# Kernel tuning notes

Measured on AMD Instinct MI355X. Metric: run time of the kernel, lower is better.

The kernel has to match this reference:

```python
import jax, jax.numpy as jnp
import numpy as np

B, T, D, H = 2, 2048, 1024, 16
HD = D // H  # head_dim = 64

def setup_inputs() -> dict:
    key = jax.random.key(0)
    ks = jax.random.split(key, 5)
    s = 0.02
    return {
        "x": jax.random.normal(ks[0], (B, T, D), dtype=jnp.float32),
        "w_qkv": jax.random.normal(ks[1], (3 * D, D), dtype=jnp.float32) * s,
        "b_qkv": jax.random.normal(ks[2], (3 * D,), dtype=jnp.float32) * s,
        "w_proj": jax.random.normal(ks[3], (D, D), dtype=jnp.float32) * s,
        "b_proj": jax.random.normal(ks[4], (D,), dtype=jnp.float32) * s,
    }

def reference(x, w_qkv, b_qkv, w_proj, b_proj):
    b, t, c = x.shape
    h, hd = H, HD
    scale = hd ** -0.5
    # qkv projection (torch Linear: x @ W^T + b)
    qkv = x @ w_qkv.T + b_qkv                      # [b, t, 3c]
    q, k, v = jnp.split(qkv, 3, axis=-1)
    # b t (h d) -> b h t d
    reshape = lambda z: z.reshape(b, t, h, hd).transpose(0, 2, 1, 3)
    q, k, v = reshape(q), reshape(k), reshape(v)
    scores = jnp.einsum("bhqd,bhkd->bhqk", q, k) * scale  # [b, h, t, t]
    causal = jnp.triu(jnp.ones((t, t), dtype=bool), k=1)   # True above diag
    scores = jnp.where(causal[None, None], -jnp.inf, scores)
    attn = jax.nn.softmax(scores, axis=-1)
    out = jnp.einsum("bhqk,bhkd->bhqd", attn, v)            # [b, h, t, d]
    out = out.transpose(0, 2, 1, 3).reshape(b, t, c)        # b h t d -> b t (h d)
    return out @ w_proj.T + b_proj
```

## Files before the change

### kernel.cpp

```cpp
#include <hip/hip_runtime.h>
#include <hip/hip_bf16.h>

#define Bq 2
#define Tq 2048
#define Dq 1024
#define Hq 16
#define HDq 64

typedef __attribute__((ext_vector_type(8))) short short8;
typedef __attribute__((ext_vector_type(4))) float f32x4;

__device__ __forceinline__ unsigned short f2bf(float f) {
  union { float f; unsigned int i; } v; v.f = f;
  unsigned int r = v.i + 0x7fffu + ((v.i >> 16) & 1u);
  return (unsigned short)(r >> 16);
}
__device__ __forceinline__ unsigned short f2bf_fast(float f) {
  union { float f; unsigned int i; } v; v.f = f;
  return (unsigned short)((v.i + 0x8000u) >> 16);
}

__device__ __forceinline__ short8 cvt8(const float* __restrict__ g) {
  const float4* gp = (const float4*)g;
  float4 x0 = gp[0], x1 = gp[1];
  short8 v;
  v[0] = (short)f2bf(x0.x); v[1] = (short)f2bf(x0.y);
  v[2] = (short)f2bf(x0.z); v[3] = (short)f2bf(x0.w);
  v[4] = (short)f2bf(x1.x); v[5] = (short)f2bf(x1.y);
  v[6] = (short)f2bf(x1.z); v[7] = (short)f2bf(x1.w);
  return v;
}

__device__ __forceinline__ void async_cp16(const void* g, void* l) {
  __builtin_amdgcn_global_load_lds(
      (const __attribute__((address_space(1))) void*)g,
      (__attribute__((address_space(3))) void*)l, 16, 0, 0);
}

constexpr int NXC = (Bq * Tq * Dq) / 8;
constexpr int NW1C = (3 * Dq * Dq) / 8;
constexpr int NW2C = (Dq * Dq) / 8;

__global__ __launch_bounds__(256)
void cvt_all(const float* __restrict__ x, const float* __restrict__ w1,
             const float* __restrict__ w2, unsigned short* __restrict__ xo,
             unsigned short* __restrict__ w1o, unsigned short* __restrict__ w2o)
{
  int i = blockIdx.x * 256 + threadIdx.x;
  const float* src; unsigned short* dst; int j;
  if (i < NXC)              { src = x;  dst = xo;  j = i; }
  else if (i < NXC + NW1C)  { src = w1; dst = w1o; j = i - NXC; }
  else                      { src = w2; dst = w2o; j = i - NXC - NW1C; }
  *(short8*)&dst[(size_t)j * 8] = cvt8(src + (size_t)j * 8);
}

template<int EPI, int BN_>
__global__ __launch_bounds__(256)
void gemm_bt(const unsigned short* __restrict__ Ab, const unsigned short* __restrict__ Wb,
             const float* __restrict__ bias, float* __restrict__ outp,
             int K, int N,
             unsigned short* __restrict__ qo, unsigned short* __restrict__ ko,
             unsigned short* __restrict__ vo)
{
  constexpr int WN = BN_ / 2;
  constexpr int NJ = WN / 16;
  constexpr int NAI = 4;
  constexpr int NBI = BN_ / 32;
  __shared__ unsigned short As[2][2 * 128 * 32];
  __shared__ unsigned short Bs[2][2 * BN_ * 32];

  const int t = threadIdx.x;
  const int lane = t & 63, w = t >> 6;
  const int m0 = blockIdx.y * 128, n0 = blockIdx.x * BN_;
  const int fr = lane & 15, qd = lane >> 4;
  const int wm = (w >> 1) * 64, wn = (w & 1) * WN;

  f32x4 acc[4][NJ] = {};
  const int NIT = K / 64;

  #pragma unroll
  for (int j = 0; j < NAI; j++) {
    int G = j * 256 + t;
    int panel = G >> 9, rowg = (G >> 2) & 127, colg = G & 3;
    async_cp16(Ab + (size_t)(m0 + rowg) * K + panel * 32 + colg * 8, &As[0][G * 8]);
  }
  #pragma unroll
  for (int j = 0; j < NBI; j++) {
    int G = j * 256 + t;
    int panel = G / (BN_ * 4), rowg = (G / 4) % BN_, colg = G & 3;
    async_cp16(Wb + (size_t)(n0 + rowg) * K + panel * 32 + colg * 8, &Bs[0][G * 8]);
  }

  for (int i = 0; i < NIT; i++) {
    const int cur = i & 1;
    __syncthreads();
    if (i + 1 < NIT) {
      const int nxt = cur ^ 1;
      const int k0 = (i + 1) * 64;
      #pragma unroll
      for (int j = 0; j < NAI; j++) {
        int G = j * 256 + t;
        int panel = G >> 9, rowg = (G >> 2) & 127, colg = G & 3;
        async_cp16(Ab + (size_t)(m0 + rowg) * K + k0 + panel * 32 + colg * 8, &As[nxt][G * 8]);
      }
      #pragma unroll
      for (int j = 0; j < NBI; j++) {
        int G = j * 256 + t;
        int panel = G / (BN_ * 4), rowg = (G / 4) % BN_, colg = G & 3;
        async_cp16(Wb + (size_t)(n0 + rowg) * K + k0 + panel * 32 + colg * 8, &Bs[nxt][G * 8]);
      }
    }
    #pragma unroll
    for (int kh = 0; kh < 2; kh++) {
      short8 af[4], bf[NJ];
      #pragma unroll
      for (int ib = 0; ib < 4; ib++)
        af[ib] = *(const short8*)&As[cur][kh * 4096 + (wm + ib * 16 + fr) * 32 + qd * 8];
      #pragma unroll
      for (int jb = 0; jb < NJ; jb++)
        bf[jb] = *(const short8*)&Bs[cur][kh * (BN_ * 32) + (wn + jb * 16 + fr) * 32 + qd * 8];
      #pragma unroll
      for (int ib = 0; ib < 4; ib++)
        #pragma unroll
        for (int jb = 0; jb < NJ; jb++)
          acc[ib][jb] = __builtin_amdgcn_mfma_f32_16x16x32_bf16(af[ib], bf[jb], acc[ib][jb], 0, 0, 0);
    }
  }

  #pragma unroll
  for (int jb = 0; jb < NJ; jb++) {
    int col = n0 + wn + jb * 16 + fr;
    float bv = bias[col];
    if (EPI == 0) {
      int which = col >> 10;
      int rem = col & 1023;
      int hh = rem >> 6, dd = rem & 63;
      #pragma unroll
      for (int ib = 0; ib < 4; ib++) {
        int row4 = m0 + wm + ib * 16 + qd * 4;
        int bb = row4 >> 11, tt = row4 & (Tq - 1);
        if (which == 2) {
          unsigned lo = (unsigned)f2bf(acc[ib][jb][0] + bv)
                      | ((unsigned)f2bf(acc[ib][jb][1] + bv) << 16);
          unsigned hi = (unsigned)f2bf(acc[ib][jb][2] + bv)
                      | ((unsigned)f2bf(acc[ib][jb][3] + bv) << 16);
          uint2 pk; pk.x = lo; pk.y = hi;
          *(uint2*)&vo[((size_t)(bb * Hq + hh) * HDq + dd) * Tq + tt] = pk;
        } else {
          unsigned short* dst = (which == 0) ? qo : ko;
          #pragma unroll
          for (int r = 0; r < 4; r++)
            dst[((size_t)(bb * Hq + hh) * Tq + tt + r) * HDq + dd] = f2bf(acc[ib][jb][r] + bv);
        }
      }
    } else {
      #pragma unroll
      for (int ib = 0; ib < 4; ib++)
        #pragma unroll
        for (int r = 0; r < 4; r++) {
          int row = m0 + wm + ib * 16 + qd * 4 + r;
          outp[(size_t)row * N + col] = acc[ib][jb][r] + bv;
        }
    }
  }
}

constexpr int AP = 72;

template<bool DIAG>
__device__ __forceinline__ void strip_one(
    const short8 aq0, const short8 aq1,
    const short8 (&bk)[4][2], const short8 (&bv)[4][2], const short8 ones,
    unsigned short* __restrict__ PsRow, int fr, int qd, int qbase,
    f32x4 (&oacc)[4], f32x4& lacc, float SCL)
{
  f32x4 s4[4] = {};
  #pragma unroll
  for (int nb = 0; nb < 4; nb++) {
    s4[nb] = __builtin_amdgcn_mfma_f32_16x16x32_bf16(aq0, bk[nb][0], s4[nb], 0, 0, 0);
    s4[nb] = __builtin_amdgcn_mfma_f32_16x16x32_bf16(aq1, bk[nb][1], s4[nb], 0, 0, 0);
  }
  #pragma unroll
  for (int nb = 0; nb < 4; nb++)
    #pragma unroll
    for (int reg = 0; reg < 4; reg++) {
      float pv = exp2f(s4[nb][reg] * SCL);
      if (DIAG && (nb * 16 + fr) > (qbase + reg)) pv = 0.f;
      PsRow[(qd * 4 + reg) * AP + nb * 16 + fr] = f2bf_fast(pv);
    }
  short8 ap0 = *(const short8*)&PsRow[fr * AP + qd * 8];
  short8 ap1 = *(const short8*)&PsRow[fr * AP + 32 + qd * 8];
  lacc = __builtin_amdgcn_mfma_f32_16x16x32_bf16(ap0, ones, lacc, 0, 0, 0);
  lacc = __builtin_amdgcn_mfma_f32_16x16x32_bf16(ap1, ones, lacc, 0, 0, 0);
  #pragma unroll
  for (int db = 0; db < 4; db++) {
    oacc[db] = __builtin_amdgcn_mfma_f32_16x16x32_bf16(ap0, bv[db][0], oacc[db], 0, 0, 0);
    oacc[db] = __builtin_amdgcn_mfma_f32_16x16x32_bf16(ap1, bv[db][1], oacc[db], 0, 0, 0);
  }
}

template<bool SMALLDIAG>
__device__ __forceinline__ void strip_dual(
    const short8 (&aqB)[2], const short8 (&aqA)[2],
    const short8 (&bk)[4][2], const short8 (&bv)[4][2], const short8 ones,
    unsigned short* __restrict__ PsB, unsigned short* __restrict__ PsA,
    int fr, int qd, int qbase,
    f32x4 (&oB)[4], f32x4& lB, f32x4 (&oA)[4], f32x4& lA, float SCL)
{
  f32x4 sB[4] = {}, sA[4] = {};
  #pragma unroll
  for (int nb = 0; nb < 4; nb++) {
    sB[nb] = __builtin_amdgcn_mfma_f32_16x16x32_bf16(aqB[0], bk[nb][0], sB[nb], 0, 0, 0);
    sA[nb] = __builtin_amdgcn_mfma_f32_16x16x32_bf16(aqA[0], bk[nb][0], sA[nb], 0, 0, 0);
  }
  #pragma unroll
  for (int nb = 0; nb < 4; nb++) {
    sB[nb] = __builtin_amdgcn_mfma_f32_16x16x32_bf16(aqB[1], bk[nb][1], sB[nb], 0, 0, 0);
    sA[nb] = __builtin_amdgcn_mfma_f32_16x16x32_bf16(aqA[1], bk[nb][1], sA[nb], 0, 0, 0);
  }
  #pragma unroll
  for (int nb = 0; nb < 4; nb++)
    #pragma unroll
    for (int reg = 0; reg < 4; reg++) {
      float pvB = exp2f(sB[nb][reg] * SCL);
      float pvA = exp2f(sA[nb][reg] * SCL);
      if (SMALLDIAG && (nb * 16 + fr) > (qbase + reg)) pvA = 0.f;
      PsB[(qd * 4 + reg) * AP + nb * 16 + fr] = f2bf_fast(pvB);
      PsA[(qd * 4 + reg) * AP + nb * 16 + fr] = f2bf_fast(pvA);
    }
  short8 apB0 = *(const short8*)&PsB[fr * AP + qd * 8];
  short8 apB1 = *(const short8*)&PsB[fr * AP + 32 + qd * 8];
  short8 apA0 = *(const short8*)&PsA[fr * AP + qd * 8];
  short8 apA1 = *(const short8*)&PsA[fr * AP + 32 + qd * 8];
  lB = __builtin_amdgcn_mfma_f32_16x16x32_bf16(apB0, ones, lB, 0, 0, 0);
  lA = __builtin_amdgcn_mfma_f32_16x16x32_bf16(apA0, ones, lA, 0, 0, 0);
  lB = __builtin_amdgcn_mfma_f32_16x16x32_bf16(apB1, ones, lB, 0, 0, 0);
  lA = __builtin_amdgcn_mfma_f32_16x16x32_bf16(apA1, ones, lA, 0, 0, 0);
  #pragma unroll
  for (int db = 0; db < 4; db++) {
    oB[db] = __builtin_amdgcn_mfma_f32_16x16x32_bf16(apB0, bv[db][0], oB[db], 0, 0, 0);
    oA[db] = __builtin_amdgcn_mfma_f32_16x16x32_bf16(apA0, bv[db][0], oA[db], 0, 0, 0);
  }
  #pragma unroll
  for (int db = 0; db < 4; db++) {
    oB[db] = __builtin_amdgcn_mfma_f32_16x16x32_bf16(apB1, bv[db][1], oB[db], 0, 0, 0);
    oA[db] = __builtin_amdgcn_mfma_f32_16x16x32_bf16(apA1, bv[db][1], oA[db], 0, 0, 0);
  }
}

__global__ __launch_bounds__(256, 2)
void attn_fwd(const unsigned short* __restrict__ qb, const unsigned short* __restrict__ kb,
              const unsigned short* __restrict__ vtb, unsigned short* __restrict__ ab)
{
  __shared__ unsigned short Ks[2][64 * 64];
  __shared__ unsigned short Vts[2][64 * 64];
  __shared__ unsigned short Ps[128 * AP];

  const int t = threadIdx.x, w = t >> 6, lane = t & 63;
  const int fr = lane & 15, qd = lane >> 4;
  const int p = blockIdx.x;
  const int bh = blockIdx.y;
  const int sB = 31 - p;
  const int sA = p;
  const int s0t[2] = { sB * 64, sA * 64 };
  const int ktB = sB;
  const int qbase = w * 16 + qd * 4;

  short8 aq[2][2];
  #pragma unroll
  for (int tl = 0; tl < 2; tl++) {
    const unsigned short* Qg = qb + ((size_t)bh * Tq + s0t[tl]) * HDq;
    #pragma unroll
    for (int c = 0; c < 2; c++)
      aq[tl][c] = *(const short8*)(Qg + (w * 16 + fr) * 64 + c * 32 + qd * 8);
  }

  const unsigned short* Kbh = kb + (size_t)bh * Tq * HDq;
  const unsigned short* Vbh = vtb + (size_t)bh * HDq * Tq;

  const int off0 = ((qd ^ (fr & 7)) * 8);
  const int off1 = off0 ^ 32;

  const int G0 = 2 * w * 64 + lane, G1 = G0 + 64;
  const int r0 = G0 >> 3, g0 = (G0 & 7) ^ (r0 & 7);
  const int r1 = G1 >> 3, g1 = (G1 & 7) ^ (r1 & 7);

  short8 ones;
  #pragma unroll
  for (int j = 0; j < 8; j++) ones[j] = (short)0x3F80;

  f32x4 oacc[2][4] = {};
  f32x4 lacc[2] = {};
  const float SCL = 0.125f * 1.44269504088896f;

  unsigned short* PsB = &Ps[(0 * 64 + w * 16) * AP];
  unsigned short* PsA = &Ps[(1 * 64 + w * 16) * AP];

  async_cp16(Kbh + (size_t)r0 * 64 + g0 * 8, &Ks[0][G0 * 8]);
  async_cp16(Vbh + (size_t)r0 * Tq + g0 * 8, &Vts[0][G0 * 8]);
  async_cp16(Kbh + (size_t)r1 * 64 + g1 * 8, &Ks[0][G1 * 8]);
  async_cp16(Vbh + (size_t)r1 * Tq + g1 * 8, &Vts[0][G1 * 8]);

  for (int kt = 0; kt <= ktB; kt++) {
    const int cur = kt & 1;
    __syncthreads();
    if (kt < ktB) {
      const int nxt = cur ^ 1;
      const size_t kofs = (size_t)(kt + 1) * 64;
      async_cp16(Kbh + (kofs + r0) * 64 + g0 * 8, &Ks[nxt][G0 * 8]);
      async_cp16(Vbh + (size_t)r0 * Tq + kofs + g0 * 8, &Vts[nxt][G0 * 8]);
      async_cp16(Kbh + (kofs + r1) * 64 + g1 * 8, &Ks[nxt][G1 * 8]);
      async_cp16(Vbh + (size_t)r1 * Tq + kofs + g1 * 8, &Vts[nxt][G1 * 8]);
    }

    short8 bk[4][2], bv[4][2];
    #pragma unroll
    for (int nb = 0; nb < 4; nb++) {
      bk[nb][0] = *(const short8*)&Ks[cur][(nb * 16 + fr) * 64 + off0];
      bk[nb][1] = *(const short8*)&Ks[cur][(nb * 16 + fr) * 64 + off1];
      bv[nb][0] = *(const short8*)&Vts[cur][(nb * 16 + fr) * 64 + off0];
      bv[nb][1] = *(const short8*)&Vts[cur][(nb * 16 + fr) * 64 + off1];
    }

    if (kt < sA) {
      strip_dual<false>(aq[0], aq[1], bk, bv, ones, PsB, PsA, fr, qd, qbase,
                        oacc[0], lacc[0], oacc[1], lacc[1], SCL);
    } else if (kt == sA) {
      strip_dual<true >(aq[0], aq[1], bk, bv, ones, PsB, PsA, fr, qd, qbase,
                        oacc[0], lacc[0], oacc[1], lacc[1], SCL);
    } else if (kt == ktB) {
      strip_one<true >(aq[0][0], aq[0][1], bk, bv, ones, PsB, fr, qd, qbase,
                       oacc[0], lacc[0], SCL);
    } else {
      strip_one<false>(aq[0][0], aq[0][1], bk, bv, ones, PsB, fr, qd, qbase,
                       oacc[0], lacc[0], SCL);
    }
  }

  #pragma unroll
  for (int tl = 0; tl < 2; tl++)
    #pragma unroll
    for (int reg = 0; reg < 4; reg++) {
      float linv = 1.0f / lacc[tl][reg];
      size_t rowoff = ((size_t)(bh >> 4) * Tq + s0t[tl] + w * 16 + qd * 4 + reg) * Dq
                    + (bh & 15) * HDq;
      #pragma unroll
      for (int db = 0; db < 4; db++)
        ab[rowoff + db * 16 + fr] = f2bf(oacc[tl][db][reg] * linv);
    }
}

extern "C" void kernel_launch(void* const* d_in, const int* in_sizes, int n_in,
                              void* d_out, int out_size, void* d_ws, size_t ws_size,
                              hipStream_t stream) {
  const float* x      = (const float*)d_in[0];
  const float* w_qkv  = (const float*)d_in[1];
  const float* b_qkv  = (const float*)d_in[2];
  const float* w_proj = (const float*)d_in[3];
  const float* b_proj = (const float*)d_in[4];
  float* out = (float*)d_out;

  unsigned short* ws = (unsigned short*)d_ws;
  const size_t NE = (size_t)Bq * Hq * Tq * HDq;
  unsigned short* qb  = ws;
  unsigned short* kb  = ws + NE;
  unsigned short* vtb = ws + 2 * NE;
  unsigned short* ab  = ws + 3 * NE;
  unsigned short* xb  = ws + 4 * NE;
  unsigned short* wqb = xb + (size_t)NXC * 8;
  unsigned short* wpb = wqb + (size_t)NW1C * 8;

  dim3 blk(256);
  cvt_all<<<dim3((NXC + NW1C + NW2C) >> 8), blk, 0, stream>>>(x, w_qkv, w_proj, xb, wqb, wpb);

  dim3 g1(3 * Dq / 128, Bq * Tq / 128);
  gemm_bt<0, 128><<<g1, blk, 0, stream>>>(xb, wqb, b_qkv, nullptr,
                                          Dq, 3 * Dq, qb, kb, vtb);
  dim3 g2(16, Bq * Hq);
  attn_fwd<<<g2, blk, 0, stream>>>(qb, kb, vtb, ab);
  dim3 g3(Dq / 64, Bq * Tq / 128);
  gemm_bt<1, 64><<<g3, blk, 0, stream>>>(ab, wpb, b_proj, out,
                                         Dq, Dq, nullptr, nullptr, nullptr);
}
```

Before: 198.3 us.

## Drop GEMM double buffering and parameterize M tile; retile output projection

```diff
diff --git a/kernel.cpp b/kernel.cpp
--- a/kernel.cpp
+++ b/kernel.cpp
@@ -54,7 +54,7 @@
   *(short8*)&dst[(size_t)j * 8] = cvt8(src + (size_t)j * 8);
 }
 
-template<int EPI, int BN_>
+template<int EPI, int BM_, int BN_>
 __global__ __launch_bounds__(256)
 void gemm_bt(const unsigned short* __restrict__ Ab, const unsigned short* __restrict__ Wb,
              const float* __restrict__ bias, float* __restrict__ outp,
@@ -62,65 +62,48 @@
              unsigned short* __restrict__ qo, unsigned short* __restrict__ ko,
              unsigned short* __restrict__ vo)
 {
-  constexpr int WN = BN_ / 2;
+  constexpr int WM = BM_ / 2, WN = BN_ / 2;
+  constexpr int NI = WM / 16;
   constexpr int NJ = WN / 16;
-  constexpr int NAI = 4;
+  constexpr int NAI = BM_ / 32;
   constexpr int NBI = BN_ / 32;
-  __shared__ unsigned short As[2][2 * 128 * 32];
-  __shared__ unsigned short Bs[2][2 * BN_ * 32];
+  __shared__ unsigned short As[2 * BM_ * 32];
+  __shared__ unsigned short Bs[2 * BN_ * 32];
 
   const int t = threadIdx.x;
   const int lane = t & 63, w = t >> 6;
-  const int m0 = blockIdx.y * 128, n0 = blockIdx.x * BN_;
+  const int m0 = blockIdx.y * BM_, n0 = blockIdx.x * BN_;
   const int fr = lane & 15, qd = lane >> 4;
-  const int wm = (w >> 1) * 64, wn = (w & 1) * WN;
-
-  f32x4 acc[4][NJ] = {};
-  const int NIT = K / 64;
-
-  #pragma unroll
-  for (int j = 0; j < NAI; j++) {
-    int G = j * 256 + t;
-    int panel = G >> 9, rowg = (G >> 2) & 127, colg = G & 3;
-    async_cp16(Ab + (size_t)(m0 + rowg) * K + panel * 32 + colg * 8, &As[0][G * 8]);
-  }
-  #pragma unroll
-  for (int j = 0; j < NBI; j++) {
-    int G = j * 256 + t;
-    int panel = G / (BN_ * 4), rowg = (G / 4) % BN_, colg = G & 3;
-    async_cp16(Wb + (size_t)(n0 + rowg) * K + panel * 32 + colg * 8, &Bs[0][G * 8]);
-  }
-
-  for (int i = 0; i < NIT; i++) {
-    const int cur = i & 1;
+  const int wm = (w >> 1) * WM, wn = (w & 1) * WN;
+
+  f32x4 acc[NI][NJ] = {};
+
+  for (int k0 = 0; k0 < K; k0 += 64) {
     __syncthreads();
-    if (i + 1 < NIT) {
-      const int nxt = cur ^ 1;
-      const int k0 = (i + 1) * 64;
-      #pragma unroll
-      for (int j = 0; j < NAI; j++) {
-        int G = j * 256 + t;
-        int panel = G >> 9, rowg = (G >> 2) & 127, colg = G & 3;
-        async_cp16(Ab + (size_t)(m0 + rowg) * K + k0 + panel * 32 + colg * 8, &As[nxt][G * 8]);
-      }
-      #pragma unroll
-      for (int j = 0; j < NBI; j++) {
-        int G = j * 256 + t;
-        int panel = G / (BN_ * 4), rowg = (G / 4) % BN_, colg = G & 3;
-        async_cp16(Wb + (size_t)(n0 + rowg) * K + k0 + panel * 32 + colg * 8, &Bs[nxt][G * 8]);
-      }
-    }
+    #pragma unroll
+    for (int j = 0; j < NAI; j++) {
+      int G = j * 256 + t;
+      int panel = G / (BM_ * 4), rowg = (G / 4) % BM_, colg = G & 3;
+      async_cp16(Ab + (size_t)(m0 + rowg) * K + k0 + panel * 32 + colg * 8, &As[G * 8]);
+    }
+    #pragma unroll
+    for (int j = 0; j < NBI; j++) {
+      int G = j * 256 + t;
+      int panel = G / (BN_ * 4), rowg = (G / 4) % BN_, colg = G & 3;
+      async_cp16(Wb + (size_t)(n0 + rowg) * K + k0 + panel * 32 + colg * 8, &Bs[G * 8]);
+    }
+    __syncthreads();
     #pragma unroll
     for (int kh = 0; kh < 2; kh++) {
-      short8 af[4], bf[NJ];
-      #pragma unroll
-      for (int ib = 0; ib < 4; ib++)
-        af[ib] = *(const short8*)&As[cur][kh * 4096 + (wm + ib * 16 + fr) * 32 + qd * 8];
+      short8 af[NI], bf[NJ];
+      #pragma unroll
+      for (int ib = 0; ib < NI; ib++)
+        af[ib] = *(const short8*)&As[kh * (BM_ * 32) + (wm + ib * 16 + fr) * 32 + qd * 8];
       #pragma unroll
       for (int jb = 0; jb < NJ; jb++)
-        bf[jb] = *(const short8*)&Bs[cur][kh * (BN_ * 32) + (wn + jb * 16 + fr) * 32 + qd * 8];
-      #pragma unroll
-      for (int ib = 0; ib < 4; ib++)
+        bf[jb] = *(const short8*)&Bs[kh * (BN_ * 32) + (wn + jb * 16 + fr) * 32 + qd * 8];
+      #pragma unroll
+      for (int ib = 0; ib < NI; ib++)
         #pragma unroll
         for (int jb = 0; jb < NJ; jb++)
           acc[ib][jb] = __builtin_amdgcn_mfma_f32_16x16x32_bf16(af[ib], bf[jb], acc[ib][jb], 0, 0, 0);
@@ -136,7 +119,7 @@
       int rem = col & 1023;
       int hh = rem >> 6, dd = rem & 63;
       #pragma unroll
-      for (int ib = 0; ib < 4; ib++) {
+      for (int ib = 0; ib < NI; ib++) {
         int row4 = m0 + wm + ib * 16 + qd * 4;
         int bb = row4 >> 11, tt = row4 & (Tq - 1);
         if (which == 2) {
@@ -155,7 +138,7 @@
       }
     } else {
       #pragma unroll
-      for (int ib = 0; ib < 4; ib++)
+      for (int ib = 0; ib < NI; ib++)
         #pragma unroll
         for (int r = 0; r < 4; r++) {
           int row = m0 + wm + ib * 16 + qd * 4 + r;
@@ -374,11 +357,11 @@
   cvt_all<<<dim3((NXC + NW1C + NW2C) >> 8), blk, 0, stream>>>(x, w_qkv, w_proj, xb, wqb, wpb);
 
   dim3 g1(3 * Dq / 128, Bq * Tq / 128);
-  gemm_bt<0, 128><<<g1, blk, 0, stream>>>(xb, wqb, b_qkv, nullptr,
-                                          Dq, 3 * Dq, qb, kb, vtb);
+  gemm_bt<0, 128, 128><<<g1, blk, 0, stream>>>(xb, wqb, b_qkv, nullptr,
+                                               Dq, 3 * Dq, qb, kb, vtb);
   dim3 g2(16, Bq * Hq);
   attn_fwd<<<g2, blk, 0, stream>>>(qb, kb, vtb, ab);
-  dim3 g3(Dq / 64, Bq * Tq / 128);
-  gemm_bt<1, 64><<<g3, blk, 0, stream>>>(ab, wpb, b_proj, out,
-                                         Dq, Dq, nullptr, nullptr, nullptr);
-}
+  dim3 g3(Dq / 128, Bq * Tq / 64);
+  gemm_bt<1, 64, 128><<<g3, blk, 0, stream>>>(ab, wpb, b_proj, out,
+                                              Dq, Dq, nullptr, nullptr, nullptr);
+}
```

Measured after the change: 188.9 us. -4.7%, faster.
